# Optimization experiments

Measured on AMD Instinct MI355X. Metric: run time of the kernel, lower is better.

## Reference

```python
import jax, jax.numpy as jnp
import numpy as np

EPS = 1e-6
START, END, FACTOR = 2.0, 8.0, 0.5


def layer_norm(x, w, b):
    mu = jnp.mean(x, axis=-1, keepdims=True)
    var = jnp.mean(jnp.square(x - mu), axis=-1, keepdims=True)
    return (x - mu) * jax.lax.rsqrt(var + EPS) * w + b


def build_spread_vector(hsize):
    # decay_i = factor ** (1 / k_i), k_i linearly spaced in [start, end]
    return FACTOR ** (1.0 / jnp.linspace(START, END, hsize, dtype=jnp.float32))


def decay_scan(decay, u):
    # cx[t] = decay * cx[t-1] + u[t], along axis 1 (seq). decay: [H], u: [B,S,H]
    a = jnp.broadcast_to(decay, u.shape)

    def combine(c1, c2):
        a1, b1 = c1
        a2, b2 = c2
        return a1 * a2, a2 * b1 + b2

    _, cx = jax.lax.associative_scan(combine, (a, u), axis=1)
    return cx


def setup_inputs() -> dict:
    key = jax.random.key(0)
    ks = jax.random.split(key, 4)
    B, S, D = 8, 2048, 1024
    sd = 1.0 / np.sqrt(D)
    return {
        "x": jax.random.normal(ks[0], (B, S, D), jnp.float32),
        "Wt": jax.random.normal(ks[1], (D, D), jnp.float32) * sd,
        "Wo": jax.random.normal(ks[2], (D, D), jnp.float32) * sd,
        "Wg": jax.random.normal(ks[3], (2 * D, D), jnp.float32) * sd,
        "bg": jnp.zeros((D,), jnp.float32),
        "ln1_w": jnp.ones((D,), jnp.float32),
        "ln1_b": jnp.zeros((D,), jnp.float32),
        "lnc_w": jnp.ones((D,), jnp.float32),
        "lnc_b": jnp.zeros((D,), jnp.float32),
        "lng_w": jnp.ones((D,), jnp.float32),
        "lng_b": jnp.zeros((D,), jnp.float32),
    }


def reference(x, Wt, Wo, Wg, bg, ln1_w, ln1_b, lnc_w, lnc_b, lng_w, lng_b):
    H = Wt.shape[1]
    decay = build_spread_vector(H)            # [H]
    decay_beta = 1.0 - decay
    _x = layer_norm(x, ln1_w, ln1_b)          # [B,S,D]
    u = jnp.einsum("bsd,dh->bsh", _x, Wt) * decay_beta
    cx = decay_scan(decay, u)                 # [B,S,H]
    out = jnp.einsum("bsh,hd->bsd", layer_norm(cx, lnc_w, lnc_b), Wo)
    res = _x                                  # norm_residual=True
    gate = jax.nn.sigmoid(
        layer_norm(jnp.concatenate((res, out), axis=-1) @ Wg + bg, lng_w, lng_b)
    )
    return (1.0 - gate) * res + gate * out
```

## Files before the change

kernel.cpp:

```cpp
#include <hip/hip_runtime.h>
#include <hip/hip_bf16.h>
#include <cmath>
#include <cstdint>

namespace {

constexpr int kB = 8;
constexpr int kS = 2048;
constexpr int kD = 1024;
constexpr int kN = kB * kS;
constexpr int kChunk = 128;
constexpr int kNChunk = kS / kChunk;
constexpr float kEps = 1e-6f;

typedef __attribute__((ext_vector_type(8))) short bf16x8;
typedef __attribute__((ext_vector_type(4))) float f32x4;

__device__ inline float bf2f(short s) {
  union { unsigned u; float f; } c;
  c.u = ((unsigned)(unsigned short)s) << 16;
  return c.f;
}

struct bh4 { __hip_bfloat16 a, b, c, d; };

__device__ inline void gload16(const void* g, void* l) {
  __builtin_amdgcn_global_load_lds(
      (const __attribute__((address_space(1))) void*)g,
      (__attribute__((address_space(3))) void*)l, 16, 0, 0);
}

__device__ inline void blockReduce2(float& s1, float& s2) {
#pragma unroll
  for (int off = 32; off > 0; off >>= 1) {
    s1 += __shfl_down(s1, off);
    s2 += __shfl_down(s2, off);
  }
  __shared__ float r1[4], r2[4];
  int wid = threadIdx.x >> 6;
  if ((threadIdx.x & 63) == 0) { r1[wid] = s1; r2[wid] = s2; }
  __syncthreads();
  s1 = r1[0] + r1[1] + r1[2] + r1[3];
  s2 = r2[0] + r2[1] + r2[2] + r2[3];
}

__global__ __launch_bounds__(256) void k_prep_ln(
    const float* __restrict__ x, const float* __restrict__ ln1w,
    const float* __restrict__ ln1b, __hip_bfloat16* __restrict__ xnb,
    const float* __restrict__ Wt, const float* __restrict__ Wo,
    const float* __restrict__ Wg, __hip_bfloat16* __restrict__ WtT,
    __hip_bfloat16* __restrict__ WoT, __hip_bfloat16* __restrict__ WgT,
    float* __restrict__ decay, float* __restrict__ dbeta,
    float* __restrict__ aL) {
  int b = blockIdx.x;
  int t = threadIdx.x;
  if (b < kN) {
    int row = b;
    const float4 v = reinterpret_cast<const float4*>(x + (size_t)row * kD)[t];
    float s1 = v.x + v.y + v.z + v.w;
    float s2 = v.x * v.x + v.y * v.y + v.z * v.z + v.w * v.w;
    blockReduce2(s1, s2);
    float mu = s1 * (1.0f / kD);
    float var = s2 * (1.0f / kD) - mu * mu;
    float rs = rsqrtf(var + kEps);
    float4 wv = reinterpret_cast<const float4*>(ln1w)[t];
    float4 bv = reinterpret_cast<const float4*>(ln1b)[t];
    bh4 o;
    o.a = __float2bfloat16((v.x - mu) * rs * wv.x + bv.x);
    o.b = __float2bfloat16((v.y - mu) * rs * wv.y + bv.y);
    o.c = __float2bfloat16((v.z - mu) * rs * wv.z + bv.z);
    o.d = __float2bfloat16((v.w - mu) * rs * wv.w + bv.w);
    reinterpret_cast<bh4*>(xnb + (size_t)row * kD)[t] = o;
    return;
  }
  b -= kN;
  if (b < 4) {
    int h = b * 256 + t;
    float kk = 2.0f + 6.0f * (float)h / (float)(kD - 1);
    float d = exp2f(-1.0f / kk);
    decay[h] = d;
    dbeta[h] = 1.0f - d;
    aL[h] = exp2f(-(float)kChunk / kk);
    return;
  }
  b -= 4;
  const float* W;
  __hip_bfloat16* WT;
  int K, local;
  if (b < 1024)      { W = Wt; WT = WtT; K = kD;     local = b; }
  else if (b < 2048) { W = Wo; WT = WoT; K = kD;     local = b - 1024; }
  else               { W = Wg; WT = WgT; K = 2 * kD; local = b - 2048; }
  int n0 = (local & 31) * 32, k0 = (local >> 5) * 32;
  __shared__ float tile[32][33];
  int tr = t >> 3, tc4 = (t & 7) * 4;
  float4 v = *reinterpret_cast<const float4*>(W + (size_t)(k0 + tr) * kD + n0 + tc4);
  tile[tc4 + 0][tr] = v.x;
  tile[tc4 + 1][tr] = v.y;
  tile[tc4 + 2][tr] = v.z;
  tile[tc4 + 3][tr] = v.w;
  __syncthreads();
  bh4 o;
  o.a = __float2bfloat16(tile[tr][tc4 + 0]);
  o.b = __float2bfloat16(tile[tr][tc4 + 1]);
  o.c = __float2bfloat16(tile[tr][tc4 + 2]);
  o.d = __float2bfloat16(tile[tr][tc4 + 3]);
  *reinterpret_cast<bh4*>(WT + (size_t)(n0 + tr) * K + k0 + tc4) = o;
}

__global__ __launch_bounds__(256) void k_ln_bf16in(
    const __hip_bfloat16* __restrict__ x, const float* __restrict__ w,
    const float* __restrict__ b, __hip_bfloat16* __restrict__ y) {
  int row = blockIdx.x;
  int t = threadIdx.x;
  short4 q = reinterpret_cast<const short4*>(x + (size_t)row * kD)[t];
  float vv[4] = {bf2f(q.x), bf2f(q.y), bf2f(q.z), bf2f(q.w)};
  float s1 = vv[0] + vv[1] + vv[2] + vv[3];
  float s2 = vv[0] * vv[0] + vv[1] * vv[1] + vv[2] * vv[2] + vv[3] * vv[3];
  blockReduce2(s1, s2);
  float mu = s1 * (1.0f / kD);
  float var = s2 * (1.0f / kD) - mu * mu;
  float rs = rsqrtf(var + kEps);
  float4 wv = reinterpret_cast<const float4*>(w)[t];
  float4 bv = reinterpret_cast<const float4*>(b)[t];
  bh4 o;
  o.a = __float2bfloat16((vv[0] - mu) * rs * wv.x + bv.x);
  o.b = __float2bfloat16((vv[1] - mu) * rs * wv.y + bv.y);
  o.c = __float2bfloat16((vv[2] - mu) * rs * wv.z + bv.z);
  o.d = __float2bfloat16((vv[3] - mu) * rs * wv.w + bv.w);
  reinterpret_cast<bh4*>(y + (size_t)row * kD)[t] = o;
}

__global__ __launch_bounds__(512, 2) void k_mfma_gemm(
    const __hip_bfloat16* __restrict__ A1, const __hip_bfloat16* __restrict__ A2,
    const __hip_bfloat16* __restrict__ BT, int K,
    float* __restrict__ C, __hip_bfloat16* __restrict__ Cb,
    const float* __restrict__ colscale, const float* __restrict__ bias,
    float* __restrict__ ends, const float* __restrict__ decay) {
  __shared__ short As[2][2][8192];
  __shared__ short Bs[2][2][8192];
  const int t = threadIdx.x;
  const int wid = t >> 6, lane = t & 63;
  const int nwg = gridDim.x;
  const int bid = blockIdx.x;
  const int s = (bid & 7) * (nwg >> 3) + (bid >> 3);
  const int bn = (s & 3) * 256;
  const int bm = (s >> 2) * 256;
  const int wr = wid >> 2;
  const int wcn = wid & 3;
  const int r = lane & 15, kg = lane >> 4;
  const int NT = K / 64;

  const int srow = lane >> 3;
  const int scol = (((lane & 7) ^ srow)) * 8;

  auto stageA = [&](int kt, int h) {
    const __hip_bfloat16* Asrc = A1;
    int kk = kt * 64;
    if (A2 && kk >= kD) { Asrc = A2; kk -= kD; }
    short* dst = &As[kt & 1][h][0];
#pragma unroll
    for (int j = 0; j < 2; ++j) {
      int chunk = wid * 2 + j;
      int row = chunk * 8 + srow;
      gload16(Asrc + (size_t)(bm + h * 128 + row) * kD + kk + scol,
              dst + chunk * 512 + lane * 8);
    }
  };
  auto stageB = [&](int kt, int h) {
    short* dst = &Bs[kt & 1][h][0];
#pragma unroll
    for (int j = 0; j < 2; ++j) {
      int chunk = wid * 2 + j;
      int row = chunk * 8 + srow;
      gload16(BT + (size_t)(bn + h * 128 + row) * K + kt * 64 + scol,
              dst + chunk * 512 + lane * 8);
    }
  };

  f32x4 acc[8][4];
#pragma unroll
  for (int m = 0; m < 8; ++m)
#pragma unroll
    for (int n = 0; n < 4; ++n) acc[m][n] = (f32x4){0.f, 0.f, 0.f, 0.f};

  stageA(0, 0); stageA(0, 1); stageB(0, 0); stageB(0, 1);
  stageB(1, 0); stageB(1, 1);
  asm volatile("s_waitcnt vmcnt(4)" ::: "memory");
  __builtin_amdgcn_s_barrier();
  asm volatile("" ::: "memory");

  for (int T = 0; T < NT; ++T) {
    const int bc = T & 1;
    const char* Ab = reinterpret_cast<const char*>(&As[bc][wr][0]);
    const char* Bb = reinterpret_cast<const char*>(&Bs[bc][wcn >> 1][0]);
    const int bcol = (wcn & 1) * 64;
    bf16x8 bfr[4][2], aLO[4][2], aHI[4][2];
#pragma unroll
    for (int n = 0; n < 4; ++n)
#pragma unroll
      for (int ks = 0; ks < 2; ++ks) {
        int row = bcol + n * 16 + r;
        int slot = (ks * 4 + kg) ^ (r & 7);
        bfr[n][ks] = *reinterpret_cast<const bf16x8*>(Bb + row * 128 + slot * 16);
      }
#pragma unroll
    for (int mm = 0; mm < 4; ++mm)
#pragma unroll
      for (int ks = 0; ks < 2; ++ks) {
        int row = mm * 16 + r;
        int slot = (ks * 4 + kg) ^ (r & 7);
        aLO[mm][ks] = *reinterpret_cast<const bf16x8*>(Ab + row * 128 + slot * 16);
      }
    if (T + 1 < NT) { stageA(T + 1, 0); stageA(T + 1, 1); }
    asm volatile("" ::: "memory");
    __builtin_amdgcn_s_barrier();
    asm volatile("" ::: "memory");
    __builtin_amdgcn_s_setprio(1);
#pragma unroll
    for (int mm = 0; mm < 4; ++mm)
#pragma unroll
      for (int n = 0; n < 4; ++n)
#pragma unroll
        for (int ks = 0; ks < 2; ++ks)
          acc[mm][n] = __builtin_amdgcn_mfma_f32_16x16x32_bf16(
              aLO[mm][ks], bfr[n][ks], acc[mm][n], 0, 0, 0);
    __builtin_amdgcn_s_setprio(0);
    asm volatile("" ::: "memory");
    __builtin_amdgcn_s_barrier();
    asm volatile("" ::: "memory");
#pragma unroll
    for (int mm = 0; mm < 4; ++mm)
#pragma unroll
      for (int ks = 0; ks < 2; ++ks) {
        int row = (mm + 4) * 16 + r;
        int slot = (ks * 4 + kg) ^ (r & 7);
        aHI[mm][ks] = *reinterpret_cast<const bf16x8*>(Ab + row * 128 + slot * 16);
      }
    if (T + 2 < NT) { stageB(T + 2, 0); stageB(T + 2, 1); }
    asm volatile("" ::: "memory");
    __builtin_amdgcn_s_barrier();
    asm volatile("" ::: "memory");
    __builtin_amdgcn_s_setprio(1);
#pragma unroll
    for (int mm = 0; mm < 4; ++mm)
#pragma unroll
      for (int n = 0; n < 4; ++n)
#pragma unroll
        for (int ks = 0; ks < 2; ++ks)
          acc[mm + 4][n] = __builtin_amdgcn_mfma_f32_16x16x32_bf16(
              aHI[mm][ks], bfr[n][ks], acc[mm + 4][n], 0, 0, 0);
    __builtin_amdgcn_s_setprio(0);
    if (T + 2 < NT)
      asm volatile("s_waitcnt vmcnt(4)" ::: "memory");
    else if (T + 1 < NT)
      asm volatile("s_waitcnt vmcnt(0)" ::: "memory");
    asm volatile("" ::: "memory");
    __builtin_amdgcn_s_barrier();
    asm volatile("" ::: "memory");
  }

  int col[4];
  float cs[4], bi[4];
#pragma unroll
  for (int n = 0; n < 4; ++n) {
    col[n] = bn + wcn * 64 + n * 16 + r;
    cs[n] = colscale ? colscale[col[n]] : 1.0f;
    bi[n] = bias ? bias[col[n]] : 0.0f;
  }
#pragma unroll
  for (int m = 0; m < 8; ++m) {
#pragma unroll
    for (int j = 0; j < 4; ++j) {
      int row = bm + wr * 128 + m * 16 + kg * 4 + j;
#pragma unroll
      for (int n = 0; n < 4; ++n) {
        float v = acc[m][n][j] * cs[n] + bi[n];
        if (C) C[(size_t)row * kD + col[n]] = v;
        if (Cb) Cb[(size_t)row * kD + col[n]] = __float2bfloat16(v);
      }
    }
  }

  if (ends) {
    const int row0 = bm + wr * 128;
    const int eidx = (row0 >> 7) * kD;
#pragma unroll
    for (int n = 0; n < 4; ++n) {
      float a = decay[col[n]];
      float a2 = a * a, a4 = a2 * a2, a8 = a4 * a4, a16 = a8 * a8;
      float pw = (kg == 3) ? 1.0f
               : (kg == 2) ? a4
               : (kg == 1) ? a4 * a4
                           : a4 * a4 * a4;
      float w[4];
      w[3] = pw;
      w[2] = pw * a;
      w[1] = pw * a2;
      w[0] = pw * a2 * a;
      float p = 0.f;
#pragma unroll
      for (int m = 7; m >= 0; --m) {
#pragma unroll
        for (int j = 0; j < 4; ++j)
          p += w[j] * (acc[m][n][j] * cs[n] + bi[n]);
#pragma unroll
        for (int j = 0; j < 4; ++j) w[j] *= a16;
      }
      p += __shfl_xor(p, 16);
      p += __shfl_xor(p, 32);
      if (kg == 0) ends[eidx + col[n]] = p;
    }
  }
}

__global__ __launch_bounds__(256) void k_scan_carry(
    const float* __restrict__ ends, const float* __restrict__ aL,
    float* __restrict__ carry) {
  int tid = blockIdx.x * blockDim.x + threadIdx.x;
  int h = tid & (kD - 1);
  int b = tid >> 10;
  float al = aL[h];
  float car = 0.f;
#pragma unroll
  for (int c = 0; c < kNChunk; ++c) {
    size_t idx = ((size_t)(b * kNChunk + c)) * kD + h;
    carry[idx] = car;
    car = fmaf(al, car, ends[idx]);
  }
}

__global__ __launch_bounds__(256) void k_scan_apply(
    __hip_bfloat16* __restrict__ u, const float* __restrict__ decay,
    const float* __restrict__ carry) {
  int tid = blockIdx.x * blockDim.x + threadIdx.x;
  int h = tid & (kD - 1);
  int c = (tid >> 10) & (kNChunk - 1);
  int b = tid >> 14;
  float a = decay[h];
  float v = carry[tid];
  __hip_bfloat16* up = u + ((size_t)(b * kS) + (size_t)c * kChunk) * kD + h;
#pragma unroll 8
  for (int i = 0; i < kChunk; ++i) {
    v = fmaf(a, v, bf2f(*(const short*)(up + (size_t)i * kD)));
    up[(size_t)i * kD] = __float2bfloat16(v);
  }
}

__global__ __launch_bounds__(256) void k_final(
    const __hip_bfloat16* __restrict__ gpre, const __hip_bfloat16* __restrict__ res,
    const __hip_bfloat16* __restrict__ outp, const float* __restrict__ w,
    const float* __restrict__ b, float* __restrict__ y) {
  int row = blockIdx.x;
  int t = threadIdx.x;
  short4 q = reinterpret_cast<const short4*>(gpre + (size_t)row * kD)[t];
  float vv[4] = {bf2f(q.x), bf2f(q.y), bf2f(q.z), bf2f(q.w)};
  float s1 = vv[0] + vv[1] + vv[2] + vv[3];
  float s2 = vv[0] * vv[0] + vv[1] * vv[1] + vv[2] * vv[2] + vv[3] * vv[3];
  blockReduce2(s1, s2);
  float mu = s1 * (1.0f / kD);
  float var = s2 * (1.0f / kD) - mu * mu;
  float rs = rsqrtf(var + kEps);
  float4 wv = reinterpret_cast<const float4*>(w)[t];
  float4 bv = reinterpret_cast<const float4*>(b)[t];
  short4 r4 = reinterpret_cast<const short4*>(res + (size_t)row * kD)[t];
  short4 o4 = reinterpret_cast<const short4*>(outp + (size_t)row * kD)[t];
  float rr[4] = {bf2f(r4.x), bf2f(r4.y), bf2f(r4.z), bf2f(r4.w)};
  float oo[4] = {bf2f(o4.x), bf2f(o4.y), bf2f(o4.z), bf2f(o4.w)};
  float ww[4] = {wv.x, wv.y, wv.z, wv.w};
  float bb[4] = {bv.x, bv.y, bv.z, bv.w};
  float4 out;
  float* op = &out.x;
#pragma unroll
  for (int i = 0; i < 4; ++i) {
    float z = (vv[i] - mu) * rs * ww[i] + bb[i];
    float g = 1.0f / (1.0f + expf(-z));
    op[i] = rr[i] + g * (oo[i] - rr[i]);
  }
  reinterpret_cast<float4*>(y + (size_t)row * kD)[t] = out;
}

}

extern "C" void kernel_launch(void* const* d_in, const int* in_sizes, int n_in,
                              void* d_out, int out_size, void* d_ws,
                              size_t ws_size, hipStream_t stream) {
  const float* x = (const float*)d_in[0];
  const float* Wt = (const float*)d_in[1];
  const float* Wo = (const float*)d_in[2];
  const float* Wg = (const float*)d_in[3];
  const float* bg = (const float*)d_in[4];
  const float* ln1w = (const float*)d_in[5];
  const float* ln1b = (const float*)d_in[6];
  const float* lncw = (const float*)d_in[7];
  const float* lncb = (const float*)d_in[8];
  const float* lngw = (const float*)d_in[9];
  const float* lngb = (const float*)d_in[10];
  float* y = (float*)d_out;

  char* ws = (char*)d_ws;
  size_t off = 0;
  auto alloc = [&](size_t bytes) {
    char* p = ws + off;
    off += (bytes + 255) & ~(size_t)255;
    return p;
  };
  __hip_bfloat16* xnb = (__hip_bfloat16*)alloc((size_t)kN * kD * 2);
  __hip_bfloat16* ub = (__hip_bfloat16*)alloc((size_t)kN * kD * 2);
  __hip_bfloat16* outb = (__hip_bfloat16*)alloc((size_t)kN * kD * 2);
  __hip_bfloat16* cxn = (__hip_bfloat16*)alloc((size_t)kN * kD * 2);
  __hip_bfloat16* WtT = (__hip_bfloat16*)alloc((size_t)kD * kD * 2);
  __hip_bfloat16* WoT = (__hip_bfloat16*)alloc((size_t)kD * kD * 2);
  __hip_bfloat16* WgT = (__hip_bfloat16*)alloc((size_t)kD * 2 * kD * 2);
  float* decay = (float*)alloc(kD * 4);
  float* dbeta = (float*)alloc(kD * 4);
  float* aL = (float*)alloc(kD * 4);
  float* ends = (float*)alloc((size_t)kB * kNChunk * kD * 4);
  float* carry = (float*)alloc((size_t)kB * kNChunk * kD * 4);

  const int nwg = (kD / 256) * (kN / 256);

  k_prep_ln<<<kN + 4 + 4096, 256, 0, stream>>>(
      x, ln1w, ln1b, xnb, Wt, Wo, Wg, WtT, WoT, WgT, decay, dbeta, aL);
  k_mfma_gemm<<<nwg, 512, 0, stream>>>(xnb, nullptr, WtT, kD, nullptr, ub,
                                       dbeta, nullptr, ends, decay);
  k_scan_carry<<<(kB * kD) / 256, 256, 0, stream>>>(ends, aL, carry);
  k_scan_apply<<<(kB * kNChunk * kD) / 256, 256, 0, stream>>>(ub, decay, carry);
  k_ln_bf16in<<<kN, 256, 0, stream>>>(ub, lncw, lncb, cxn);
  k_mfma_gemm<<<nwg, 512, 0, stream>>>(cxn, nullptr, WoT, kD, nullptr, outb,
                                       nullptr, nullptr, nullptr, nullptr);
  k_mfma_gemm<<<nwg, 512, 0, stream>>>(xnb, outb, WgT, 2 * kD, nullptr, ub,
                                       nullptr, bg, nullptr, nullptr);
  k_final<<<kN, 256, 0, stream>>>(ub, xnb, outb, lngw, lngb, y);
}
```

Baseline: 222.7 us.

## Fuse chunked decay-scan apply with LayerNorm and shrink scan chunks

The scan-apply pass and the following LayerNorm kernel become one kernel. Each block walks 32 consecutive rows of one chunk, carrying the recurrence state for 4 channels per thread and normalising each row in place, so the bf16 intermediate is no longer written and re-read. The chunk size drops from 128 to 32 to give enough blocks, so the GEMM epilogue now emits four chunk-end partial sums per wave and the carry pass has more serial steps. The cost is a block-wide reduction with barriers on every row of a serial loop. A trailing barrier is added to the reduction so it can be called repeatedly.

```diff
diff --git a/kernel.cpp b/kernel.cpp
--- a/kernel.cpp
+++ b/kernel.cpp
@@ -9,7 +9,7 @@
 constexpr int kS = 2048;
 constexpr int kD = 1024;
 constexpr int kN = kB * kS;
-constexpr int kChunk = 128;
+constexpr int kChunk = 32;
 constexpr int kNChunk = kS / kChunk;
 constexpr float kEps = 1e-6f;
 
@@ -42,6 +42,7 @@
   __syncthreads();
   s1 = r1[0] + r1[1] + r1[2] + r1[3];
   s2 = r2[0] + r2[1] + r2[2] + r2[3];
+  __syncthreads();
 }
 
 __global__ __launch_bounds__(256) void k_prep_ln(
@@ -107,29 +108,6 @@
   *reinterpret_cast<bh4*>(WT + (size_t)(n0 + tr) * K + k0 + tc4) = o;
 }
 
-__global__ __launch_bounds__(256) void k_ln_bf16in(
-    const __hip_bfloat16* __restrict__ x, const float* __restrict__ w,
-    const float* __restrict__ b, __hip_bfloat16* __restrict__ y) {
-  int row = blockIdx.x;
-  int t = threadIdx.x;
-  short4 q = reinterpret_cast<const short4*>(x + (size_t)row * kD)[t];
-  float vv[4] = {bf2f(q.x), bf2f(q.y), bf2f(q.z), bf2f(q.w)};
-  float s1 = vv[0] + vv[1] + vv[2] + vv[3];
-  float s2 = vv[0] * vv[0] + vv[1] * vv[1] + vv[2] * vv[2] + vv[3] * vv[3];
-  blockReduce2(s1, s2);
-  float mu = s1 * (1.0f / kD);
-  float var = s2 * (1.0f / kD) - mu * mu;
-  float rs = rsqrtf(var + kEps);
-  float4 wv = reinterpret_cast<const float4*>(w)[t];
-  float4 bv = reinterpret_cast<const float4*>(b)[t];
-  bh4 o;
-  o.a = __float2bfloat16((vv[0] - mu) * rs * wv.x + bv.x);
-  o.b = __float2bfloat16((vv[1] - mu) * rs * wv.y + bv.y);
-  o.c = __float2bfloat16((vv[2] - mu) * rs * wv.z + bv.z);
-  o.d = __float2bfloat16((vv[3] - mu) * rs * wv.w + bv.w);
-  reinterpret_cast<bh4*>(y + (size_t)row * kD)[t] = o;
-}
-
 __global__ __launch_bounds__(512, 2) void k_mfma_gemm(
     const __hip_bfloat16* __restrict__ A1, const __hip_bfloat16* __restrict__ A2,
     const __hip_bfloat16* __restrict__ BT, int K,
@@ -283,7 +261,7 @@
 
   if (ends) {
     const int row0 = bm + wr * 128;
-    const int eidx = (row0 >> 7) * kD;
+    const int chunk0 = row0 >> 5;
 #pragma unroll
     for (int n = 0; n < 4; ++n) {
       float a = decay[col[n]];
@@ -292,23 +270,21 @@
                : (kg == 2) ? a4
                : (kg == 1) ? a4 * a4
                            : a4 * a4 * a4;
-      float w[4];
-      w[3] = pw;
-      w[2] = pw * a;
-      w[1] = pw * a2;
-      w[0] = pw * a2 * a;
-      float p = 0.f;
-#pragma unroll
-      for (int m = 7; m >= 0; --m) {
-#pragma unroll
-        for (int j = 0; j < 4; ++j)
-          p += w[j] * (acc[m][n][j] * cs[n] + bi[n]);
-#pragma unroll
-        for (int j = 0; j < 4; ++j) w[j] *= a16;
+      float v3 = pw, v2 = pw * a, v1 = pw * a2, v0 = pw * a2 * a;
+      const float vj[4] = {v0, v1, v2, v3};
+#pragma unroll
+      for (int c2 = 0; c2 < 4; ++c2) {
+        float p = 0.f;
+#pragma unroll
+        for (int j = 0; j < 4; ++j) {
+          float u0 = acc[2 * c2][n][j] * cs[n] + bi[n];
+          float u1 = acc[2 * c2 + 1][n][j] * cs[n] + bi[n];
+          p += vj[j] * (a16 * u0 + u1);
+        }
+        p += __shfl_xor(p, 16);
+        p += __shfl_xor(p, 32);
+        if (kg == 0) ends[(size_t)(chunk0 + c2) * kD + col[n]] = p;
       }
-      p += __shfl_xor(p, 16);
-      p += __shfl_xor(p, 32);
-      if (kg == 0) ends[eidx + col[n]] = p;
     }
   }
 }
@@ -329,20 +305,42 @@
   }
 }
 
-__global__ __launch_bounds__(256) void k_scan_apply(
-    __hip_bfloat16* __restrict__ u, const float* __restrict__ decay,
-    const float* __restrict__ carry) {
-  int tid = blockIdx.x * blockDim.x + threadIdx.x;
-  int h = tid & (kD - 1);
-  int c = (tid >> 10) & (kNChunk - 1);
-  int b = tid >> 14;
-  float a = decay[h];
-  float v = carry[tid];
-  __hip_bfloat16* up = u + ((size_t)(b * kS) + (size_t)c * kChunk) * kD + h;
-#pragma unroll 8
+__global__ __launch_bounds__(256) void k_scan_apply_ln(
+    const __hip_bfloat16* __restrict__ u, const float* __restrict__ decay,
+    const float* __restrict__ carry, const float* __restrict__ lnw,
+    const float* __restrict__ lnb, __hip_bfloat16* __restrict__ cxn) {
+  const int blk = blockIdx.x;
+  const int t = threadIdx.x;
+  const int h0 = t * 4;
+  const int b = blk >> 6, c = blk & 63;
+  const size_t rowbase = (size_t)b * kS + (size_t)c * kChunk;
+
+  float a0 = decay[h0], a1 = decay[h0 + 1], a2 = decay[h0 + 2],
+        a3 = decay[h0 + 3];
+  const float4 cv = *reinterpret_cast<const float4*>(
+      carry + (size_t)blk * kD + h0);
+  float v0 = cv.x, v1 = cv.y, v2 = cv.z, v3 = cv.w;
+  const float4 wv = *reinterpret_cast<const float4*>(lnw + h0);
+  const float4 bv = *reinterpret_cast<const float4*>(lnb + h0);
+
   for (int i = 0; i < kChunk; ++i) {
-    v = fmaf(a, v, bf2f(*(const short*)(up + (size_t)i * kD)));
-    up[(size_t)i * kD] = __float2bfloat16(v);
+    short4 q = *reinterpret_cast<const short4*>(u + (rowbase + i) * kD + h0);
+    v0 = fmaf(a0, v0, bf2f(q.x));
+    v1 = fmaf(a1, v1, bf2f(q.y));
+    v2 = fmaf(a2, v2, bf2f(q.z));
+    v3 = fmaf(a3, v3, bf2f(q.w));
+    float s1 = v0 + v1 + v2 + v3;
+    float s2 = v0 * v0 + v1 * v1 + v2 * v2 + v3 * v3;
+    blockReduce2(s1, s2);
+    float mu = s1 * (1.0f / kD);
+    float var = s2 * (1.0f / kD) - mu * mu;
+    float rs = rsqrtf(var + kEps);
+    bh4 o;
+    o.a = __float2bfloat16((v0 - mu) * rs * wv.x + bv.x);
+    o.b = __float2bfloat16((v1 - mu) * rs * wv.y + bv.y);
+    o.c = __float2bfloat16((v2 - mu) * rs * wv.z + bv.z);
+    o.d = __float2bfloat16((v3 - mu) * rs * wv.w + bv.w);
+    *reinterpret_cast<bh4*>(cxn + (rowbase + i) * kD + h0) = o;
   }
 }
 
@@ -424,8 +422,8 @@
   k_mfma_gemm<<<nwg, 512, 0, stream>>>(xnb, nullptr, WtT, kD, nullptr, ub,
                                        dbeta, nullptr, ends, decay);
   k_scan_carry<<<(kB * kD) / 256, 256, 0, stream>>>(ends, aL, carry);
-  k_scan_apply<<<(kB * kNChunk * kD) / 256, 256, 0, stream>>>(ub, decay, carry);
-  k_ln_bf16in<<<kN, 256, 0, stream>>>(ub, lncw, lncb, cxn);
+  k_scan_apply_ln<<<kB * kNChunk, 256, 0, stream>>>(ub, decay, carry, lncw,
+                                                    lncb, cxn);
   k_mfma_gemm<<<nwg, 512, 0, stream>>>(cxn, nullptr, WoT, kD, nullptr, outb,
                                        nullptr, nullptr, nullptr, nullptr);
   k_mfma_gemm<<<nwg, 512, 0, stream>>>(xnb, outb, WgT, 2 * kD, nullptr, ub,
```

Measured after the change: 225.8 us. Within noise of the previous version (+1.4%).
